# Kernel tuning notes

Measured on AMD Instinct MI355X. Metric: run time of the kernel, lower is better.

Reference implementation:

```python
import jax, jax.numpy as jnp
import numpy as np

N = 50000          # nodes
E = 1600000        # edges (before self-loops)
DIN = 128
HEADS = (8, 8, 4)
FEATS = (16, 16, 16)
NEG_SLOPE = 0.2


def setup_inputs() -> dict:
    key = jax.random.key(0)
    ks = jax.random.split(key, 2 + 4 * 3)
    inp = {
        "X": jax.random.normal(ks[0], (N, DIN), dtype=jnp.float32),
        "A": jax.random.randint(ks[1], (2, E), 0, N, dtype=jnp.int32),
    }
    in_dims = [DIN, HEADS[0] * FEATS[0], HEADS[1] * FEATS[1]]
    k = 2
    for i, (h, f) in enumerate(zip(HEADS, FEATS)):
        din = in_dims[i]
        concat = i + 1 < len(HEADS)
        inp[f"W{i+1}"] = jax.random.normal(ks[k], (din, h * f), dtype=jnp.float32) / np.float32(np.sqrt(din)); k += 1
        inp[f"as{i+1}"] = jax.random.normal(ks[k], (h, f), dtype=jnp.float32) * 0.1; k += 1
        inp[f"ad{i+1}"] = jax.random.normal(ks[k], (h, f), dtype=jnp.float32) * 0.1; k += 1
        inp[f"b{i+1}"] = jnp.zeros((h * f if concat else f,), dtype=jnp.float32); k += 1
    return inp


def _gat_conv(x, src, dst, W, a_src, a_dst, b, concat):
    # PyG-style GATConv (eval mode, self-loops already in src/dst)
    H, F = a_src.shape
    h = (x @ W).reshape(-1, H, F)                     # [N, H, F]
    e = jax.nn.leaky_relu((h * a_src).sum(-1)[src] + (h * a_dst).sum(-1)[dst], NEG_SLOPE)  # [Etot, H]
    m = jax.ops.segment_max(e, dst, num_segments=N)   # segment softmax over dst neighborhoods
    ex = jnp.exp(e - m[dst])
    s = jax.ops.segment_sum(ex, dst, num_segments=N)
    alpha = ex / (s[dst] + 1e-16)                     # [Etot, H]
    out = jax.ops.segment_sum(h[src] * alpha[:, :, None], dst, num_segments=N)  # [N, H, F]
    out = out.reshape(N, H * F) if concat else out.mean(axis=1)
    return out + b


def reference(X, A, W1, as1, ad1, b1, W2, as2, ad2, b2, W3, as3, ad3, b3):
    loops = jnp.arange(N, dtype=A.dtype)              # GATConv default add_self_loops=True
    src = jnp.concatenate([A[0], loops])
    dst = jnp.concatenate([A[1], loops])
    x = jax.nn.relu(_gat_conv(X, src, dst, W1, as1, ad1, b1, True))
    x = jax.nn.relu(_gat_conv(x, src, dst, W2, as2, ad2, b2, True))
    return _gat_conv(x, src, dst, W3, as3, ad3, b3, False)
```

## Files before the change

### kernel.cpp

```cpp
#include <hip/hip_runtime.h>
#include <hip/hip_bf16.h>

#define NN 50000
#define EE 1600000
#define DIN 128

#define BKT_SHIFT 6
#define NB ((NN + 63) >> 6)
#define BSLACK 3072
#define CHUNK 4096

typedef _Float16 half_t;
typedef __attribute__((ext_vector_type(2))) _Float16 half2_t;
typedef __attribute__((ext_vector_type(4))) _Float16 half4_t;
typedef __attribute__((ext_vector_type(8))) _Float16 half8_t;

__global__ void zero_gc(int* __restrict__ gcursor) {
    int i = blockIdx.x * 256 + threadIdx.x;
    if (i < NB) gcursor[i] = 0;
}

__global__ __launch_bounds__(256) void bin_kernel(const int* __restrict__ A,
                                                  int* __restrict__ gcursor,
                                                  int* __restrict__ binned, int e, int n) {
    __shared__ int lcount[NB];
    __shared__ int lbase[NB];
    int chunk0 = blockIdx.x * CHUNK;
    int cend = chunk0 + CHUNK;
    if (cend > e + n) cend = e + n;
    for (int i = threadIdx.x; i < NB; i += 256) lcount[i] = 0;
    __syncthreads();
    int sreg[16], dreg[16];
#pragma unroll
    for (int l = 0; l < 16; ++l) {
        int i = chunk0 + l * 256 + threadIdx.x;
        if (i < cend) {
            if (i < e) { sreg[l] = A[i]; dreg[l] = A[e + i]; }
            else       { sreg[l] = dreg[l] = i - e; }
            atomicAdd(&lcount[dreg[l] >> BKT_SHIFT], 1);
        } else {
            dreg[l] = -1;
        }
    }
    __syncthreads();
    for (int b = threadIdx.x; b < NB; b += 256) {
        int c = lcount[b];
        lbase[b] = c ? atomicAdd(&gcursor[b], c) : 0;
        lcount[b] = 0;
    }
    __syncthreads();
#pragma unroll
    for (int l = 0; l < 16; ++l) {
        if (dreg[l] >= 0) {
            int bkt = dreg[l] >> BKT_SHIFT;
            int pos = lbase[bkt] + atomicAdd(&lcount[bkt], 1);
            if (pos < BSLACK)
                binned[(size_t)bkt * BSLACK + pos] = (sreg[l] << 6) | (dreg[l] & 63);
        }
    }
}

__global__ void scan_nb(const int* __restrict__ gcursor, int* __restrict__ bbase) {
    __shared__ int s[1024];
    int t = threadIdx.x;
    int v = (t < NB) ? gcursor[t] : 0;
    s[t] = v;
    __syncthreads();
    for (int off = 1; off < 1024; off <<= 1) {
        int u = (t >= off) ? s[t - off] : 0;
        __syncthreads();
        s[t] += u;
        __syncthreads();
    }
    if (t < NB) bbase[t] = s[t] - v;
}

__global__ __launch_bounds__(256) void fine_scatter(const int* __restrict__ binned,
                                                    const int* __restrict__ gcursor,
                                                    const int* __restrict__ bbase,
                                                    int* __restrict__ indptr,
                                                    int* __restrict__ csr) {
    __shared__ int lc[64];
    __shared__ int scur[64];
    int b = blockIdx.x;
    int node0 = b << BKT_SHIFT;
    int cnt = gcursor[b];
    if (cnt > BSLACK) cnt = BSLACK;
    const int* bp = binned + (size_t)b * BSLACK;
    if (threadIdx.x < 64) lc[threadIdx.x] = 0;
    if (b == 0 && threadIdx.x == 0) indptr[NN] = EE + NN;
    __syncthreads();
    for (int j = threadIdx.x; j < cnt; j += 256) atomicAdd(&lc[bp[j] & 63], 1);
    __syncthreads();
    if (threadIdx.x < 64) {
        int lane = threadIdx.x;
        int c = lc[lane];
        int v = c;
#pragma unroll
        for (int off = 1; off < 64; off <<= 1) {
            int u = __shfl_up(v, off, 64);
            if (lane >= off) v += u;
        }
        int excl = bbase[b] + v - c;
        scur[lane] = excl;
        if (node0 + lane < NN) indptr[node0 + lane] = excl;
    }
    __syncthreads();
    for (int j = threadIdx.x; j < cnt; j += 256) {
        int v = bp[j];
        int pos = atomicAdd(&scur[v & 63], 1);
        csr[pos] = v >> 6;
    }
}

__global__ __launch_bounds__(256) void gemm_fused128(const float* __restrict__ A,
                                                     const float* __restrict__ B,
                                                     const float* __restrict__ asrc,
                                                     const float* __restrict__ adst,
                                                     half_t* __restrict__ C16,
                                                     float* __restrict__ ss,
                                                     float* __restrict__ ds, int M) {
    __shared__ float As[32][65];
    __shared__ float Bs[32][128];
    int tid = threadIdx.x;
    int tcol = tid & 15, trow = tid >> 4;
    int row0 = blockIdx.x * 64;
    float acc[4][8] = {};

    for (int k0 = 0; k0 < 128; k0 += 32) {
#pragma unroll
        for (int l = 0; l < 2; ++l) {
            int id = tid + l * 256;
            int r = id >> 3, c4 = (id & 7) * 4;
            int grow = row0 + r;
            float4 v = make_float4(0.f, 0.f, 0.f, 0.f);
            if (grow < M) v = *(const float4*)(A + (size_t)grow * 128 + k0 + c4);
            As[c4 + 0][r] = v.x;
            As[c4 + 1][r] = v.y;
            As[c4 + 2][r] = v.z;
            As[c4 + 3][r] = v.w;
        }
#pragma unroll
        for (int l = 0; l < 4; ++l) {
            int id = tid + l * 256;
            int r = id >> 5, c4 = (id & 31) * 4;
            *(float4*)(&Bs[r][c4]) = *(const float4*)(B + (size_t)(k0 + r) * 128 + c4);
        }
        __syncthreads();
#pragma unroll
        for (int k = 0; k < 32; ++k) {
            float a[4], b[8];
#pragma unroll
            for (int i = 0; i < 4; ++i) a[i] = As[k][trow * 4 + i];
#pragma unroll
            for (int j = 0; j < 8; ++j) b[j] = Bs[k][tcol * 8 + j];
#pragma unroll
            for (int i = 0; i < 4; ++i)
#pragma unroll
                for (int j = 0; j < 8; ++j) acc[i][j] += a[i] * b[j];
        }
        __syncthreads();
    }
    int hh = tcol >> 1;
    int fw0 = (tcol & 1) * 8;
#pragma unroll
    for (int i = 0; i < 4; ++i) {
        int grow = row0 + trow * 4 + i;
        float sp = 0.f, dp = 0.f;
#pragma unroll
        for (int j = 0; j < 8; ++j) {
            sp += acc[i][j] * asrc[hh * 16 + fw0 + j];
            dp += acc[i][j] * adst[hh * 16 + fw0 + j];
        }
        sp += __shfl_xor(sp, 1, 64);
        dp += __shfl_xor(dp, 1, 64);
        if (grow < M) {
            half8_t hv;
#pragma unroll
            for (int j = 0; j < 8; ++j) hv[j] = (half_t)acc[i][j];
            *(half8_t*)(C16 + (size_t)grow * 128 + tcol * 8) = hv;
            if ((tcol & 1) == 0) {
                ss[(size_t)grow * 8 + hh] = sp;
                ds[(size_t)grow * 8 + hh] = dp;
            }
        }
    }
}

__global__ __launch_bounds__(256) void gemm_fused64(const float* __restrict__ A,
                                                    const float* __restrict__ B,
                                                    const float* __restrict__ asrc,
                                                    const float* __restrict__ adst,
                                                    half_t* __restrict__ C16,
                                                    float* __restrict__ ss,
                                                    float* __restrict__ ds, int M) {
    __shared__ float As[32][65];
    __shared__ float Bs[32][64];
    int tid = threadIdx.x;
    int tx = tid & 15, ty = tid >> 4;
    int row0 = blockIdx.x * 64;
    float acc[4][4] = {};

    for (int k0 = 0; k0 < 128; k0 += 32) {
#pragma unroll
        for (int l = 0; l < 2; ++l) {
            int id = tid + l * 256;
            int r = id >> 3, c4 = (id & 7) * 4;
            int grow = row0 + r;
            float4 v = make_float4(0.f, 0.f, 0.f, 0.f);
            if (grow < M) v = *(const float4*)(A + (size_t)grow * 128 + k0 + c4);
            As[c4 + 0][r] = v.x;
            As[c4 + 1][r] = v.y;
            As[c4 + 2][r] = v.z;
            As[c4 + 3][r] = v.w;
        }
#pragma unroll
        for (int l = 0; l < 2; ++l) {
            int id = tid + l * 256;
            int r = id >> 4, c4 = (id & 15) * 4;
            *(float4*)(&Bs[r][c4]) = *(const float4*)(B + (size_t)(k0 + r) * 64 + c4);
        }
        __syncthreads();
#pragma unroll
        for (int k = 0; k < 32; ++k) {
            float a[4], b[4];
#pragma unroll
            for (int i = 0; i < 4; ++i) a[i] = As[k][ty * 4 + i];
#pragma unroll
            for (int j = 0; j < 4; ++j) b[j] = Bs[k][tx * 4 + j];
#pragma unroll
            for (int i = 0; i < 4; ++i)
#pragma unroll
                for (int j = 0; j < 4; ++j) acc[i][j] += a[i] * b[j];
        }
        __syncthreads();
    }
    int hh = tx >> 2;
    int fq = (tx & 3) * 4;
#pragma unroll
    for (int i = 0; i < 4; ++i) {
        int grow = row0 + ty * 4 + i;
        float sp = 0.f, dp = 0.f;
#pragma unroll
        for (int j = 0; j < 4; ++j) {
            sp += acc[i][j] * asrc[hh * 16 + fq + j];
            dp += acc[i][j] * adst[hh * 16 + fq + j];
        }
        sp += __shfl_xor(sp, 1, 64); sp += __shfl_xor(sp, 2, 64);
        dp += __shfl_xor(dp, 1, 64); dp += __shfl_xor(dp, 2, 64);
        if (grow < M) {
            half4_t hv;
#pragma unroll
            for (int j = 0; j < 4; ++j) hv[j] = (half_t)acc[i][j];
            *(half4_t*)(C16 + (size_t)grow * 64 + tx * 4) = hv;
            if ((tx & 3) == 0) {
                ss[(size_t)grow * 4 + hh] = sp;
                ds[(size_t)grow * 4 + hh] = dp;
            }
        }
    }
}

template <int H, int F, bool MEAN, bool RELU>
__global__ __launch_bounds__(256) void aggregate_hw(
    const half_t* __restrict__ h, const float* __restrict__ ss, const float* __restrict__ dsc_arr,
    const int* __restrict__ csr, const int* __restrict__ indptr,
    const float* __restrict__ bias, float* __restrict__ out, int n) {
    constexpr int HF = H * F;
    constexpr int FPL = HF / 32;
    int wave = blockIdx.x * (blockDim.x >> 6) + (threadIdx.x >> 6);
    int lane = threadIdx.x & 63;
    if (wave >= n) return;
    int half = lane >> 5, hl = lane & 31;
    int hf = hl * FPL;
    int hh = hf / F;
    float dsc = dsc_arr[wave * H + hh];
    int begin = indptr[wave], end = indptr[wave + 1];

    float ssum = 0.f;
    float acc[FPL];
#pragma unroll
    for (int k = 0; k < FPL; ++k) acc[k] = 0.f;

    int j = begin + half;
    for (; j + 2 < end; j += 4) {
        int s0 = csr[j], s1 = csr[j + 2];
        float e0 = ss[s0 * H + hh], e1 = ss[s1 * H + hh];
        const half_t* p0 = h + (size_t)s0 * HF + hf;
        const half_t* p1 = h + (size_t)s1 * HF + hf;
        half4_t t0, t1;
        if constexpr (FPL == 4) {
            t0 = *(const half4_t*)p0;
            t1 = *(const half4_t*)p1;
        } else {
            half2_t a0 = *(const half2_t*)p0, a1 = *(const half2_t*)p1;
            t0[0] = a0[0]; t0[1] = a0[1];
            t1[0] = a1[0]; t1[1] = a1[1];
        }
        e0 += dsc; e0 = (e0 > 0.f) ? e0 : 0.2f * e0;
        e1 += dsc; e1 = (e1 > 0.f) ? e1 : 0.2f * e1;
        float x0 = __expf(e0), x1 = __expf(e1);
        ssum += x0 + x1;
#pragma unroll
        for (int k = 0; k < FPL; ++k) {
            acc[k] = fmaf(x0, (float)t0[k], acc[k]);
            acc[k] = fmaf(x1, (float)t1[k], acc[k]);
        }
    }
    for (; j < end; j += 2) {
        int s = csr[j];
        float e = ss[s * H + hh] + dsc;
        e = (e > 0.f) ? e : 0.2f * e;
        const half_t* hp = h + (size_t)s * HF + hf;
        float x = __expf(e);
        ssum += x;
        if constexpr (FPL == 4) {
            half4_t t = *(const half4_t*)hp;
#pragma unroll
            for (int k = 0; k < 4; ++k) acc[k] = fmaf(x, (float)t[k], acc[k]);
        } else {
            half2_t t = *(const half2_t*)hp;
#pragma unroll
            for (int k = 0; k < 2; ++k) acc[k] = fmaf(x, (float)t[k], acc[k]);
        }
    }

    ssum += __shfl_xor(ssum, 32, 64);
#pragma unroll
    for (int k = 0; k < FPL; ++k) acc[k] += __shfl_xor(acc[k], 32, 64);

    float inv = 1.f / (ssum + 1e-16f);
    if (!MEAN) {
        if (half == 0) {
            float v0 = acc[0] * inv + bias[hf + 0];
            float v1 = acc[1] * inv + bias[hf + 1];
            float v2 = acc[2] * inv + bias[hf + 2];
            float v3 = acc[3] * inv + bias[hf + 3];
            if (RELU) {
                v0 = fmaxf(v0, 0.f); v1 = fmaxf(v1, 0.f);
                v2 = fmaxf(v2, 0.f); v3 = fmaxf(v3, 0.f);
            }
            *(float4*)(out + (size_t)wave * HF + hf) = make_float4(v0, v1, v2, v3);
        }
    } else {
        float val[FPL];
#pragma unroll
        for (int k = 0; k < FPL; ++k) {
            val[k] = acc[k] * inv;
            val[k] += __shfl_xor(val[k], 8, 64);
            val[k] += __shfl_xor(val[k], 16, 64);
        }
        if (lane < 8) {
            float v0 = val[0] * 0.25f + bias[hl * 2 + 0];
            float v1 = val[1] * 0.25f + bias[hl * 2 + 1];
            *(float2*)(out + (size_t)wave * F + hl * 2) = make_float2(v0, v1);
        }
    }
}

extern "C" void kernel_launch(void* const* d_in, const int* in_sizes, int n_in,
                              void* d_out, int out_size, void* d_ws, size_t ws_size,
                              hipStream_t stream) {
    const float* X  = (const float*)d_in[0];
    const int*   A  = (const int*)d_in[1];
    const float* W1 = (const float*)d_in[2];
    const float* as1 = (const float*)d_in[3];
    const float* ad1 = (const float*)d_in[4];
    const float* b1  = (const float*)d_in[5];
    const float* W2 = (const float*)d_in[6];
    const float* as2 = (const float*)d_in[7];
    const float* ad2 = (const float*)d_in[8];
    const float* b2  = (const float*)d_in[9];
    const float* W3 = (const float*)d_in[10];
    const float* as3 = (const float*)d_in[11];
    const float* ad3 = (const float*)d_in[12];
    const float* b3  = (const float*)d_in[13];

    const int N = NN, E = EE;
    const int Etot = E + N;

    char* p = (char*)d_ws;
    auto take = [&](size_t bytes) {
        char* r = p;
        p += (bytes + 255) & ~(size_t)255;
        return (void*)r;
    };
    half_t* hbuf  = (half_t*)take((size_t)N * 128 * 2);
    float* xA     = (float*)take((size_t)N * 128 * 4);
    float* xB     = (float*)take((size_t)N * 128 * 4);
    float* ssb    = (float*)take((size_t)N * 8 * 4);
    float* dsb    = (float*)take((size_t)N * 8 * 4);
    int* indptr   = (int*)take((size_t)(N + 1) * 4);
    int* gcursor  = (int*)take((size_t)NB * 4);
    int* bbase    = (int*)take((size_t)NB * 4);
    int* csr      = (int*)take((size_t)Etot * 4);
    int* binned   = (int*)xA;

    zero_gc<<<(NB + 255) / 256, 256, 0, stream>>>(gcursor);
    bin_kernel<<<(Etot + CHUNK - 1) / CHUNK, 256, 0, stream>>>(A, gcursor, binned, E, N);
    scan_nb<<<1, 1024, 0, stream>>>(gcursor, bbase);
    fine_scatter<<<NB, 256, 0, stream>>>(binned, gcursor, bbase, indptr, csr);

    const int gemmRows = (N + 63) / 64;
    const int aggBlocks = (N + 3) / 4;

    gemm_fused128<<<gemmRows, 256, 0, stream>>>(X, W1, as1, ad1, hbuf, ssb, dsb, N);
    aggregate_hw<8, 16, false, true>
        <<<aggBlocks, 256, 0, stream>>>(hbuf, ssb, dsb, csr, indptr, b1, xA, N);

    gemm_fused128<<<gemmRows, 256, 0, stream>>>(xA, W2, as2, ad2, hbuf, ssb, dsb, N);
    aggregate_hw<8, 16, false, true>
        <<<aggBlocks, 256, 0, stream>>>(hbuf, ssb, dsb, csr, indptr, b2, xB, N);

    gemm_fused64<<<gemmRows, 256, 0, stream>>>(xB, W3, as3, ad3, hbuf, ssb, dsb, N);
    aggregate_hw<4, 16, true, false>
        <<<aggBlocks, 256, 0, stream>>>(hbuf, ssb, dsb, csr, indptr, b3, (float*)d_out, N);
}
```

Measured before the change: 410.3 us.

## Drop global bucket scan using padded CSR and quarter-wave edge aggregation

The CSR build no longer runs a separate prefix-scan kernel. Each bucket keeps its fixed BSLACK-sized slot in the edge array, and per-node begin/end arrays replace indptr. BSLACK is reduced to shrink that padded buffer. The aggregation kernel now splits each wave into four 16-lane quarters, each walking a different edge. Lanes load 8 (or 4) halves per gather and the partial sums are combined with an extra shuffle stage. The aim is to cut one launch and raise memory-level parallelism and load width in the gather-bound aggregation. The cost is a larger padded CSR footprint and a greater risk of silently truncating edges when a bucket holds more than the smaller slack.

```diff
diff --git a/kernel.cpp b/kernel.cpp
--- a/kernel.cpp
+++ b/kernel.cpp
@@ -7,7 +7,7 @@
 
 #define BKT_SHIFT 6
 #define NB ((NN + 63) >> 6)
-#define BSLACK 3072
+#define BSLACK 2688
 #define CHUNK 4096
 
 typedef _Float16 half_t;
@@ -60,25 +60,10 @@
     }
 }
 
-__global__ void scan_nb(const int* __restrict__ gcursor, int* __restrict__ bbase) {
-    __shared__ int s[1024];
-    int t = threadIdx.x;
-    int v = (t < NB) ? gcursor[t] : 0;
-    s[t] = v;
-    __syncthreads();
-    for (int off = 1; off < 1024; off <<= 1) {
-        int u = (t >= off) ? s[t - off] : 0;
-        __syncthreads();
-        s[t] += u;
-        __syncthreads();
-    }
-    if (t < NB) bbase[t] = s[t] - v;
-}
-
 __global__ __launch_bounds__(256) void fine_scatter(const int* __restrict__ binned,
                                                     const int* __restrict__ gcursor,
-                                                    const int* __restrict__ bbase,
-                                                    int* __restrict__ indptr,
+                                                    int* __restrict__ begE,
+                                                    int* __restrict__ endE,
                                                     int* __restrict__ csr) {
     __shared__ int lc[64];
     __shared__ int scur[64];
@@ -88,7 +73,6 @@
     if (cnt > BSLACK) cnt = BSLACK;
     const int* bp = binned + (size_t)b * BSLACK;
     if (threadIdx.x < 64) lc[threadIdx.x] = 0;
-    if (b == 0 && threadIdx.x == 0) indptr[NN] = EE + NN;
     __syncthreads();
     for (int j = threadIdx.x; j < cnt; j += 256) atomicAdd(&lc[bp[j] & 63], 1);
     __syncthreads();
@@ -101,9 +85,13 @@
             int u = __shfl_up(v, off, 64);
             if (lane >= off) v += u;
         }
-        int excl = bbase[b] + v - c;
-        scur[lane] = excl;
-        if (node0 + lane < NN) indptr[node0 + lane] = excl;
+        int begin = b * BSLACK + v - c;
+        scur[lane] = begin;
+        int node = node0 + lane;
+        if (node < NN) {
+            begE[node] = begin;
+            endE[node] = begin + c;
+        }
     }
     __syncthreads();
     for (int j = threadIdx.x; j < cnt; j += 256) {
@@ -262,98 +250,107 @@
 }
 
 template <int H, int F, bool MEAN, bool RELU>
-__global__ __launch_bounds__(256) void aggregate_hw(
+__global__ __launch_bounds__(256) void aggregate_qw(
     const half_t* __restrict__ h, const float* __restrict__ ss, const float* __restrict__ dsc_arr,
-    const int* __restrict__ csr, const int* __restrict__ indptr,
+    const int* __restrict__ csr, const int* __restrict__ begE, const int* __restrict__ endE,
     const float* __restrict__ bias, float* __restrict__ out, int n) {
     constexpr int HF = H * F;
-    constexpr int FPL = HF / 32;
+    constexpr int FPL = HF / 16;
     int wave = blockIdx.x * (blockDim.x >> 6) + (threadIdx.x >> 6);
     int lane = threadIdx.x & 63;
     if (wave >= n) return;
-    int half = lane >> 5, hl = lane & 31;
-    int hf = hl * FPL;
+    int q = lane >> 4, ql = lane & 15;
+    int hf = ql * FPL;
     int hh = hf / F;
     float dsc = dsc_arr[wave * H + hh];
-    int begin = indptr[wave], end = indptr[wave + 1];
+    int begin = begE[wave], end = endE[wave];
 
     float ssum = 0.f;
     float acc[FPL];
 #pragma unroll
     for (int k = 0; k < FPL; ++k) acc[k] = 0.f;
 
-    int j = begin + half;
-    for (; j + 2 < end; j += 4) {
-        int s0 = csr[j], s1 = csr[j + 2];
+    int j = begin + q;
+    for (; j + 4 < end; j += 8) {
+        int s0 = csr[j], s1 = csr[j + 4];
         float e0 = ss[s0 * H + hh], e1 = ss[s1 * H + hh];
         const half_t* p0 = h + (size_t)s0 * HF + hf;
         const half_t* p1 = h + (size_t)s1 * HF + hf;
-        half4_t t0, t1;
-        if constexpr (FPL == 4) {
-            t0 = *(const half4_t*)p0;
-            t1 = *(const half4_t*)p1;
-        } else {
-            half2_t a0 = *(const half2_t*)p0, a1 = *(const half2_t*)p1;
-            t0[0] = a0[0]; t0[1] = a0[1];
-            t1[0] = a1[0]; t1[1] = a1[1];
-        }
         e0 += dsc; e0 = (e0 > 0.f) ? e0 : 0.2f * e0;
         e1 += dsc; e1 = (e1 > 0.f) ? e1 : 0.2f * e1;
         float x0 = __expf(e0), x1 = __expf(e1);
         ssum += x0 + x1;
-#pragma unroll
-        for (int k = 0; k < FPL; ++k) {
-            acc[k] = fmaf(x0, (float)t0[k], acc[k]);
-            acc[k] = fmaf(x1, (float)t1[k], acc[k]);
-        }
-    }
-    for (; j < end; j += 2) {
+        if constexpr (FPL == 8) {
+            half8_t t0 = *(const half8_t*)p0, t1 = *(const half8_t*)p1;
+#pragma unroll
+            for (int k = 0; k < 8; ++k) {
+                acc[k] = fmaf(x0, (float)t0[k], acc[k]);
+                acc[k] = fmaf(x1, (float)t1[k], acc[k]);
+            }
+        } else {
+            half4_t t0 = *(const half4_t*)p0, t1 = *(const half4_t*)p1;
+#pragma unroll
+            for (int k = 0; k < 4; ++k) {
+                acc[k] = fmaf(x0, (float)t0[k], acc[k]);
+                acc[k] = fmaf(x1, (float)t1[k], acc[k]);
+            }
+        }
+    }
+    for (; j < end; j += 4) {
         int s = csr[j];
         float e = ss[s * H + hh] + dsc;
         e = (e > 0.f) ? e : 0.2f * e;
-        const half_t* hp = h + (size_t)s * HF + hf;
         float x = __expf(e);
         ssum += x;
-        if constexpr (FPL == 4) {
+        const half_t* hp = h + (size_t)s * HF + hf;
+        if constexpr (FPL == 8) {
+            half8_t t = *(const half8_t*)hp;
+#pragma unroll
+            for (int k = 0; k < 8; ++k) acc[k] = fmaf(x, (float)t[k], acc[k]);
+        } else {
             half4_t t = *(const half4_t*)hp;
 #pragma unroll
             for (int k = 0; k < 4; ++k) acc[k] = fmaf(x, (float)t[k], acc[k]);
-        } else {
-            half2_t t = *(const half2_t*)hp;
-#pragma unroll
-            for (int k = 0; k < 2; ++k) acc[k] = fmaf(x, (float)t[k], acc[k]);
-        }
-    }
-
+        }
+    }
+
+    ssum += __shfl_xor(ssum, 16, 64);
     ssum += __shfl_xor(ssum, 32, 64);
 #pragma unroll
-    for (int k = 0; k < FPL; ++k) acc[k] += __shfl_xor(acc[k], 32, 64);
+    for (int k = 0; k < FPL; ++k) {
+        acc[k] += __shfl_xor(acc[k], 16, 64);
+        acc[k] += __shfl_xor(acc[k], 32, 64);
+    }
 
     float inv = 1.f / (ssum + 1e-16f);
-    if (!MEAN) {
-        if (half == 0) {
-            float v0 = acc[0] * inv + bias[hf + 0];
-            float v1 = acc[1] * inv + bias[hf + 1];
-            float v2 = acc[2] * inv + bias[hf + 2];
-            float v3 = acc[3] * inv + bias[hf + 3];
+    if constexpr (!MEAN) {
+        if (lane < 32) {
+            int k0 = (lane >> 4) * 4;
+            int f = (lane & 15) * FPL + k0;
+            float v0 = acc[k0 + 0] * inv + bias[f + 0];
+            float v1 = acc[k0 + 1] * inv + bias[f + 1];
+            float v2 = acc[k0 + 2] * inv + bias[f + 2];
+            float v3 = acc[k0 + 3] * inv + bias[f + 3];
             if (RELU) {
                 v0 = fmaxf(v0, 0.f); v1 = fmaxf(v1, 0.f);
                 v2 = fmaxf(v2, 0.f); v3 = fmaxf(v3, 0.f);
             }
-            *(float4*)(out + (size_t)wave * HF + hf) = make_float4(v0, v1, v2, v3);
+            *(float4*)(out + (size_t)wave * HF + f) = make_float4(v0, v1, v2, v3);
         }
     } else {
         float val[FPL];
 #pragma unroll
         for (int k = 0; k < FPL; ++k) {
             val[k] = acc[k] * inv;
+            val[k] += __shfl_xor(val[k], 4, 64);
             val[k] += __shfl_xor(val[k], 8, 64);
-            val[k] += __shfl_xor(val[k], 16, 64);
-        }
-        if (lane < 8) {
-            float v0 = val[0] * 0.25f + bias[hl * 2 + 0];
-            float v1 = val[1] * 0.25f + bias[hl * 2 + 1];
-            *(float2*)(out + (size_t)wave * F + hl * 2) = make_float2(v0, v1);
+        }
+        if (lane < 4) {
+            float v0 = val[0] * 0.25f + bias[lane * 4 + 0];
+            float v1 = val[1] * 0.25f + bias[lane * 4 + 1];
+            float v2 = val[2] * 0.25f + bias[lane * 4 + 2];
+            float v3 = val[3] * 0.25f + bias[lane * 4 + 3];
+            *(float4*)(out + (size_t)wave * F + lane * 4) = make_float4(v0, v1, v2, v3);
         }
     }
 }
@@ -390,29 +387,28 @@
     float* xB     = (float*)take((size_t)N * 128 * 4);
     float* ssb    = (float*)take((size_t)N * 8 * 4);
     float* dsb    = (float*)take((size_t)N * 8 * 4);
-    int* indptr   = (int*)take((size_t)(N + 1) * 4);
+    int* begE     = (int*)take((size_t)N * 4);
+    int* endE     = (int*)take((size_t)N * 4);
     int* gcursor  = (int*)take((size_t)NB * 4);
-    int* bbase    = (int*)take((size_t)NB * 4);
-    int* csr      = (int*)take((size_t)Etot * 4);
+    int* csr      = (int*)take((size_t)NB * BSLACK * 4);
     int* binned   = (int*)xA;
 
     zero_gc<<<(NB + 255) / 256, 256, 0, stream>>>(gcursor);
     bin_kernel<<<(Etot + CHUNK - 1) / CHUNK, 256, 0, stream>>>(A, gcursor, binned, E, N);
-    scan_nb<<<1, 1024, 0, stream>>>(gcursor, bbase);
-    fine_scatter<<<NB, 256, 0, stream>>>(binned, gcursor, bbase, indptr, csr);
+    fine_scatter<<<NB, 256, 0, stream>>>(binned, gcursor, begE, endE, csr);
 
     const int gemmRows = (N + 63) / 64;
     const int aggBlocks = (N + 3) / 4;
 
     gemm_fused128<<<gemmRows, 256, 0, stream>>>(X, W1, as1, ad1, hbuf, ssb, dsb, N);
-    aggregate_hw<8, 16, false, true>
-        <<<aggBlocks, 256, 0, stream>>>(hbuf, ssb, dsb, csr, indptr, b1, xA, N);
+    aggregate_qw<8, 16, false, true>
+        <<<aggBlocks, 256, 0, stream>>>(hbuf, ssb, dsb, csr, begE, endE, b1, xA, N);
 
     gemm_fused128<<<gemmRows, 256, 0, stream>>>(xA, W2, as2, ad2, hbuf, ssb, dsb, N);
-    aggregate_hw<8, 16, false, true>
-        <<<aggBlocks, 256, 0, stream>>>(hbuf, ssb, dsb, csr, indptr, b2, xB, N);
+    aggregate_qw<8, 16, false, true>
+        <<<aggBlocks, 256, 0, stream>>>(hbuf, ssb, dsb, csr, begE, endE, b2, xB, N);
 
     gemm_fused64<<<gemmRows, 256, 0, stream>>>(xB, W3, as3, ad3, hbuf, ssb, dsb, N);
-    aggregate_hw<4, 16, true, false>
-        <<<aggBlocks, 256, 0, stream>>>(hbuf, ssb, dsb, csr, indptr, b3, (float*)d_out, N);
-}
+    aggregate_qw<4, 16, true, false>
+        <<<aggBlocks, 256, 0, stream>>>(hbuf, ssb, dsb, csr, begE, endE, b3, (float*)d_out, N);
+}
```

New measurement: 378.6 us. 1.08x faster.
